# Optimization experiments

Hardware: AMD Instinct MI355X
Metric: run time of the kernel (lower is better)

## Reference

```python
import jax, jax.numpy as jnp
import numpy as np

N = 4096       # nodes
E = 131072     # edges (avg degree 32)
IN_C = 512
HID = 512
OUT_C = 64
RANK = 64      # svd_q
N_DOM = 4
EPS = 1e-5     # BatchNorm eps


def setup_inputs() -> dict:
    key = jax.random.key(0)
    ks = jax.random.split(key, 12)
    x = jax.random.normal(ks[0], (N, IN_C), dtype=jnp.float32)
    row = jax.random.randint(ks[1], (E,), 0, N)
    off = jax.random.randint(ks[2], (E,), 1, N)
    col = (row + off) % N  # guarantee no pre-existing self loops
    edge_index = jnp.stack([row, col]).astype(jnp.int32)
    edge_weight = jax.random.uniform(ks[3], (E,), dtype=jnp.float32)
    y = jax.random.randint(ks[4], (N,), 0, N_DOM).astype(jnp.int32)
    W1 = jax.random.normal(ks[5], (IN_C, HID), dtype=jnp.float32) / np.sqrt(IN_C).astype(np.float32)
    b1 = jnp.zeros((HID,), jnp.float32)
    Wmu = jax.random.normal(ks[6], (HID, OUT_C), dtype=jnp.float32) / np.sqrt(HID).astype(np.float32)
    bmu = jnp.zeros((OUT_C,), jnp.float32)
    Wlv = jax.random.normal(ks[7], (HID, OUT_C), dtype=jnp.float32) / np.sqrt(HID).astype(np.float32)
    blv = jnp.zeros((OUT_C,), jnp.float32)
    gamma = jnp.ones((N_DOM, HID), jnp.float32)   # per-domain BN weight
    beta = jnp.zeros((N_DOM, HID), jnp.float32)   # per-domain BN bias
    return dict(x=x, edge_index=edge_index, edge_weight=edge_weight, y=y,
                W1=W1, b1=b1, Wmu=Wmu, bmu=bmu, Wlv=Wlv, blv=blv,
                gamma=gamma, beta=beta)


def _safe_rsqrt(deg):
    # PyG gcn_norm: deg^-0.5 with inf (and here non-positive) masked to 0
    safe = jnp.where(deg > 0, deg, 1.0)
    return jnp.where(deg > 0, 1.0 / jnp.sqrt(safe), 0.0)


def gcn_conv_edges(x, W, b, row, col, w, n):
    # GCNConv with edge weights: add remaining self loops (fill=1), symmetric norm
    loop = jnp.arange(n, dtype=row.dtype)
    row_f = jnp.concatenate([row, loop])
    col_f = jnp.concatenate([col, loop])
    w_f = jnp.concatenate([w, jnp.ones((n,), w.dtype)])
    deg = jax.ops.segment_sum(w_f, col_f, num_segments=n)
    dinv = _safe_rsqrt(deg)
    norm = dinv[row_f] * w_f * dinv[col_f]
    xw = x @ W                                   # [n, out]
    out = jax.ops.segment_sum(norm[:, None] * xw[row_f], col_f, num_segments=n)
    return out + b


def gcn_conv_dense(x, W, b, A):
    # Dense-adjacency GCNConv (reconstructed adjacency already has a diagonal,
    # so add_remaining_self_loops is a no-op). deg over target (col) index.
    deg = A.sum(axis=0)
    dinv = _safe_rsqrt(deg)
    Ahat = dinv[:, None] * A * dinv[None, :]     # [n, n] normalized
    return Ahat.T @ (x @ W) + b                  # aggregate at targets


def svd_lowrank_recon(A, q, niter=2):
    # torch.svd_lowrank-style randomized SVD, then U @ diag(s) @ V^T
    omega = jax.random.normal(jax.random.key(42), (A.shape[1], q), A.dtype)
    Qb = jnp.linalg.qr(A @ omega)[0]
    for _ in range(niter):
        Qb = jnp.linalg.qr(A.T @ Qb)[0]
        Qb = jnp.linalg.qr(A @ Qb)[0]
    B = Qb.T @ A                                 # [q, n]
    U, s, Vt = jnp.linalg.svd(B, full_matrices=False)
    return (Qb @ (U * s)) @ Vt                   # [n, n] low-rank reconstruction


def dsbn_relu(x, y, gamma, beta):
    # Domain-specific BatchNorm (training-mode batch stats per domain) + ReLU
    out = jnp.zeros_like(x)
    for i in range(N_DOM):
        m = (y == i)
        mf = m.astype(x.dtype)[:, None]
        cnt = jnp.maximum(mf.sum(), 1.0)
        mean = (x * mf).sum(0) / cnt
        var = (((x - mean) ** 2) * mf).sum(0) / cnt   # biased var, as BatchNorm
        xn = (x - mean) / jnp.sqrt(var + EPS) * gamma[i] + beta[i]
        out = jnp.where(m[:, None], xn, out)
    return jax.nn.relu(out)


def reference(x, edge_index, edge_weight, y, W1, b1, Wmu, bmu, Wlv, blv, gamma, beta):
    row, col = edge_index[0], edge_index[1]
    # ----- branch 1: original sparse graph -----
    h1 = dsbn_relu(gcn_conv_edges(x, W1, b1, row, col, edge_weight, N), y, gamma, beta)
    z_mean1 = gcn_conv_edges(h1, Wmu, bmu, row, col, edge_weight, N)
    z_log1 = gcn_conv_edges(h1, Wlv, blv, row, col, edge_weight, N)
    # ----- branch 2: SVD low-rank reconstructed (dense) graph -----
    A = jnp.zeros((N, N), x.dtype).at[row, col].add(edge_weight)  # coalesced COO
    A2 = svd_lowrank_recon(A, RANK)
    h2 = dsbn_relu(gcn_conv_dense(x, W1, b1, A2), y, gamma, beta)
    z_mean2 = gcn_conv_dense(h2, Wmu, bmu, A2)
    z_log2 = gcn_conv_dense(h2, Wlv, blv, A2)
    return (z_mean1, z_log1, z_mean2, z_log2)
```

## Files before the change

kernel.cpp:

```cpp
#include <hip/hip_runtime.h>
#include <hip/hip_bf16.h>


#define NN    4096
#define NEDG  131072
#define INC   512
#define HIDC  512
#define OUTC  64
#define RK    64
#define NDOM  4
#define EPSBN 1e-5f

typedef unsigned short ushortT;
typedef __attribute__((ext_vector_type(8))) short bf16x8;
typedef __attribute__((ext_vector_type(4))) float f32x4;

static inline int cdiv(int a, int b){ return (a + b - 1) / b; }

__device__ __forceinline__ float bf2f(unsigned u){ return __uint_as_float(u << 16); }

__global__ __launch_bounds__(256) void k_detect(const unsigned short* __restrict__ p,
                                                int* __restrict__ flag){
  int t = threadIdx.x;
  int cnt = 0;
// ... 26 lines not shown
#define OFF1 (SEG_X)
#define OFF2 (OFF1+SEG_W1)
#define OFF3 (OFF2+SEG_W)
#define OFF4 (OFF3+SEG_WMU)
#define OFF5 (OFF4+SEG_WMU)
#define OFF6 (OFF5+SEG_GB)
#define OFF7 (OFF6+SEG_GB)
#define OFF8 (OFF7+SEG_B1)
#define OFF9 (OFF8+SEG_BO)
#define OFFT (OFF9+SEG_BO)

__global__ __launch_bounds__(256) void k_upcast_all(
    const void* x, const void* W1, const void* w, const void* Wmu, const void* Wlv,
    const void* gm, const void* bt, const void* b1, const void* bmu, const void* blv,
    const int* __restrict__ isf32,
    float* dx, float* dW1, float* dw, float* dWmu, float* dWlv,
    float* dgm, float* dbt, float* db1, float* dbmu, float* dblv,
    ushortT* xbf, ushortT* W1bf, ushortT* Wmubf, ushortT* Wlvbf){
  int i = blockIdx.x*256 + threadIdx.x;
  if (i >= OFFT) return;
  int f = *isf32;
  if      (i < OFF1){ float v = upc1(x, f, i); dx[i] = v; xbf[i] = tobf(v); }
  else if (i < OFF2){ float v = upc1(W1, f, i - OFF1); dW1[i - OFF1] = v; W1bf[i - OFF1] = tobf(v); }
  else if (i < OFF3) dw  [i - OFF2] = upc1(w,   f, i - OFF2);
  else if (i < OFF4){ float v = upc1(Wmu, f, i - OFF3); dWmu[i - OFF3] = v; Wmubf[i - OFF3] = tobf(v); }
  else if (i < OFF5){ float v = upc1(Wlv, f, i - OFF4); dWlv[i - OFF4] = v; Wlvbf[i - OFF4] = tobf(v); }
  else if (i < OFF6) dgm [i - OFF5] = upc1(gm,  f, i - OFF5);
  else if (i < OFF7) dbt [i - OFF6] = upc1(bt,  f, i - OFF6);
  else if (i < OFF8) db1 [i - OFF7] = upc1(b1,  f, i - OFF7);
  else if (i < OFF9) dbmu[i - OFF8] = upc1(bmu, f, i - OFF8);
  else               dblv[i - OFF9] = upc1(blv, f, i - OFF9);
}

__global__ __launch_bounds__(256) void k_fill(float* d, float v, int n){
  int i = blockIdx.x*256 + threadIdx.x;
  if (i < n) d[i] = v;
}
__global__ __launch_bounds__(256) void k_filld(double* d, double v, int n){
  int i = blockIdx.x*256 + threadIdx.x;
  if (i < n) d[i] = v;
}
__global__ __launch_bounds__(256) void k_prep(float* deg, int* cntR, int* cntC, int* dcnt){
  int i = blockIdx.x*256 + threadIdx.x;
  if (i < NN){ deg[i] = 1.0f; cntR[i] = 0; cntC[i] = 0; }
  if (i < NDOM) dcnt[i] = 0;
}
__global__ __launch_bounds__(256) void k_fin(const double* __restrict__ Qd,
        float* __restrict__ Bf1, const double* __restrict__ Cd, float* __restrict__ Cm,
        const double* __restrict__ qs, float* __restrict__ dinv2){
  int i = blockIdx.x*256 + threadIdx.x;
  if (i < NN*RK){ Bf1[i] = (float)Qd[i]; Cm[i] = (float)Cd[i]; }
  if (i < NN){
    double s = 0.0;
    #pragma unroll
    for (int k = 0; k < RK; k++) s += Cd[(size_t)i*RK + k] * qs[k];
    dinv2[i] = (s > 0.0) ? (float)(1.0/sqrt(s)) : 0.f;
  }
}

__global__ __launch_bounds__(256) void k_hist(const int* __restrict__ row, const int* __restrict__ col,
                                              const float* __restrict__ w, float* deg,
                                              int* cntR, int* cntC){
  int e = blockIdx.x*256 + threadIdx.x;
  if (e < NEDG){
    atomicAdd(&deg[col[e]], w[e]);
    atomicAdd(&cntR[row[e]], 1);
    atomicAdd(&cntC[col[e]], 1);
  }
}
__global__ __launch_bounds__(256) void k_dinv(const float* deg, float* dinv, int n){
  int i = blockIdx.x*256 + threadIdx.x;
  if (i < n){ float d = deg[i]; dinv[i] = (d > 0.f) ? 1.f/sqrtf(d) : 0.f; }
}
__global__ __launch_bounds__(256) void k_norm1(const int* __restrict__ row, const int* __restrict__ col,
                                               const float* __restrict__ w, const float* __restrict__ dinv,
                                               float* __restrict__ nrm){
  int e = blockIdx.x*256 + threadIdx.x;
  if (e < NEDG) nrm[e] = dinv[row[e]] * w[e] * dinv[col[e]];
}
__global__ __launch_bounds__(1024) void k_scan4096(const int* __restrict__ cnt,
                                                   int* __restrict__ ptr, int* __restrict__ pos){
  __shared__ int sh[1024];
  int t = threadIdx.x;
  int b = t*4;
  int a0 = cnt[b], a1 = cnt[b+1], a2 = cnt[b+2], a3 = cnt[b+3];
  sh[t] = a0 + a1 + a2 + a3;
  __syncthreads();
  for (int off = 1; off < 1024; off <<= 1){
    int v = (t >= off) ? sh[t-off] : 0;
    __syncthreads();
// ... 52 lines not shown

__device__ double erfinv64(double x){
  double w = -log1p(-x*x);
  double p;
  if (w < 5.0){
    w -= 2.5;
    p = 2.81022636e-08;  p = p*w + 3.43273939e-07; p = p*w - 3.5233877e-06;
    p = p*w - 4.39150654e-06; p = p*w + 0.00021858087; p = p*w - 0.00125372503;
    p = p*w - 0.00417768164;  p = p*w + 0.246640727;   p = p*w + 1.50140941;
  } else {
    w = sqrt(w) - 3.0;
    p = -0.000200214257; p = p*w + 0.000100950558; p = p*w + 0.00134934322;
    p = p*w - 0.00367342844; p = p*w + 0.00573950773; p = p*w - 0.0076224613;
    p = p*w + 0.00943887047; p = p*w + 1.00167406;    p = p*w + 2.83297682;
  }
  double y = p * x;
  const double c = 1.1283791670955126;
  #pragma unroll
  for (int it = 0; it < 3; it++){
    double err = erf(y) - x;
    y -= err / (c * exp(-y*y));
  }
  return y;
}

__device__ float bits_to_normal(unsigned b){
  float f = __uint_as_float((b >> 9) | 0x3f800000u) - 1.0f;
  const float lo = -0.99999994f;
  float x = fmaxf(lo, f * 2.0f + lo);
  double r = 1.4142135623730951 * erfinv64((double)x);
  return (float)r;
}

__global__ __launch_bounds__(256) void k_omega(float* __restrict__ om){
  int i = blockIdx.x*256 + threadIdx.x;
  if (i >= 262144) return;
  unsigned o0, o1;
  tf2x32(0u, 42u, 0u, (unsigned)i, &o0, &o1);
  om[i] = bits_to_normal(o0 ^ o1);
}

__global__ __launch_bounds__(256) void k_gemm_bf16(
    const ushortT* __restrict__ A, const ushortT* __restrict__ B,
    float* __restrict__ Cc, ushortT* __restrict__ Cbf){
  __shared__ ushortT As2[64][40];
  __shared__ ushortT Bs2[64][40];
  int t = threadIdx.x;
  int bm = blockIdx.y * 64, bn = blockIdx.x * 64;
  int w = t >> 6, l = t & 63;
  int lr = l & 15, lk = l >> 4;
  f32x4 acc[4] = {};
  int ar = t >> 2, ac = (t & 3) * 8;
  int bc = t & 63, bk = (t >> 6) * 8;
  for (int k0 = 0; k0 < 512; k0 += 32){
    *(uint4*)&As2[ar][ac] = *(const uint4*)&A[(size_t)(bm + ar) * 512 + k0 + ac];
    ushortT tmp[8];
    #pragma unroll
    for (int j = 0; j < 8; j++)
      tmp[j] = B[(size_t)(k0 + bk + j) * 512 + bn + bc];
    *(uint4*)&Bs2[bc][bk] = *(uint4*)tmp;
    __syncthreads();
    bf16x8 afrag = *(bf16x8*)&As2[w * 16 + lr][lk * 8];
    #pragma unroll
    for (int nt = 0; nt < 4; nt++){
      bf16x8 bfrag = *(bf16x8*)&Bs2[nt * 16 + lr][lk * 8];
      acc[nt] = __builtin_amdgcn_mfma_f32_16x16x32_bf16(afrag, bfrag, acc[nt], 0, 0, 0);
    }
    __syncthreads();
  }
  #pragma unroll
  for (int nt = 0; nt < 4; nt++){
    #pragma unroll
    for (int i = 0; i < 4; i++){
      size_t idx = (size_t)(bm + w * 16 + lk * 4 + i) * 512 + bn + nt * 16 + lr;
      float v = acc[nt][i];
      Cc[idx] = v;
      Cbf[idx] = tobf(v);
    }
  }
}

__global__ __launch_bounds__(256) void k_gemm_hw2(
    const ushortT* __restrict__ A, const ushortT* __restrict__ Bm,
    const ushortT* __restrict__ Bl, float* __restrict__ Ca, float* __restrict__ Cb){
  __shared__ ushortT As2[64][40];
  __shared__ ushortT Bs2[64][40];
  int t = threadIdx.x;
  int nb = NN/64;
  int second = blockIdx.x >= nb;
  int bm = (blockIdx.x - (second ? nb : 0)) * 64;
  const ushortT* B = second ? Bl : Bm;
  float* Cc = second ? Cb : Ca;
  int w = t >> 6, l = t & 63;
  int lr = l & 15, lk = l >> 4;
  f32x4 acc[4] = {};
  int ar = t >> 2, ac = (t & 3) * 8;
  int bc = t & 63, bk = (t >> 6) * 8;
  for (int k0 = 0; k0 < 512; k0 += 32){
    *(uint4*)&As2[ar][ac] = *(const uint4*)&A[(size_t)(bm + ar) * 512 + k0 + ac];
    ushortT tmp[8];
    #pragma unroll
    for (int j = 0; j < 8; j++)
      tmp[j] = B[(size_t)(k0 + bk + j) * 64 + bc];
    *(uint4*)&Bs2[bc][bk] = *(uint4*)tmp;
    __syncthreads();
    bf16x8 afrag = *(bf16x8*)&As2[w * 16 + lr][lk * 8];
    #pragma unroll
    for (int nt = 0; nt < 4; nt++){
      bf16x8 bfrag = *(bf16x8*)&Bs2[nt * 16 + lr][lk * 8];
      acc[nt] = __builtin_amdgcn_mfma_f32_16x16x32_bf16(afrag, bfrag, acc[nt], 0, 0, 0);
    }
    __syncthreads();
  }
  #pragma unroll
  for (int nt = 0; nt < 4; nt++){
    #pragma unroll
    for (int i = 0; i < 4; i++){
      Cc[(size_t)(bm + w * 16 + lk * 4 + i) * 64 + nt * 16 + lr] = acc[nt][i];
    }
  }
}

__global__ __launch_bounds__(256) void k_gemm_nn(int M, int Nn, int K,
      const float* __restrict__ A, int lda, const float* __restrict__ B, int ldb,
      float* __restrict__ Cc, int ldc, const float* __restrict__ rowscale,
      const float* __restrict__ kscale, const float* __restrict__ bias){
  __shared__ float As[16][65];
  __shared__ float Bs[16][65];
  int bm = blockIdx.y*64, bn = blockIdx.x*64;
  int t = threadIdx.x;
  int tr = t >> 4, tc = t & 15;
  float acc[4][4] = {};
  for (int k0 = 0; k0 < K; k0 += 16){
    #pragma unroll
    for (int q = 0; q < 4; q++){
      int idx = t*4 + q;
      int m = idx >> 4, kk = idx & 15;
      As[kk][m] = A[(size_t)(bm+m)*lda + (k0+kk)];
    }
    #pragma unroll
    for (int q = 0; q < 4; q++){
      int idx = t + q*256;
      int kk = idx >> 6, n = idx & 63;
      float ks = kscale ? kscale[k0+kk] : 1.0f;
      Bs[kk][n] = B[(size_t)(k0+kk)*ldb + (bn+n)] * ks;
    }
    __syncthreads();
    #pragma unroll
    for (int kk = 0; kk < 16; kk++){
      float a0 = As[kk][tr*4+0], a1 = As[kk][tr*4+1], a2 = As[kk][tr*4+2], a3 = As[kk][tr*4+3];
      float b0 = Bs[kk][tc*4+0], b1 = Bs[kk][tc*4+1], b2 = Bs[kk][tc*4+2], b3 = Bs[kk][tc*4+3];
      acc[0][0] += a0*b0; acc[0][1] += a0*b1; acc[0][2] += a0*b2; acc[0][3] += a0*b3;
      acc[1][0] += a1*b0; acc[1][1] += a1*b1; acc[1][2] += a1*b2; acc[1][3] += a1*b3;
      acc[2][0] += a2*b0; acc[2][1] += a2*b1; acc[2][2] += a2*b2; acc[2][3] += a2*b3;
      acc[3][0] += a3*b0; acc[3][1] += a3*b1; acc[3][2] += a3*b2; acc[3][3] += a3*b3;
    }
    __syncthreads();
  }
  #pragma unroll
  for (int i2 = 0; i2 < 4; i2++){
    int m = bm + tr*4 + i2;
    float rs = rowscale ? rowscale[m] : 1.0f;
    #pragma unroll
    for (int j2 = 0; j2 < 4; j2++){
      int n = bn + tc*4 + j2;
      float v = acc[i2][j2] * rs;
      if (bias) v += bias[n];
      Cc[(size_t)m*ldc + n] = v;
    }
  }
}

__global__ __launch_bounds__(256) void k_gemm_nn2(
      const float* __restrict__ A,
      const float* __restrict__ Um,
      const float* __restrict__ rowscale,
      const float* __restrict__ bmu, const float* __restrict__ blv,
      float* __restrict__ zout){
  __shared__ float As[16][65];
  __shared__ float Bs[16][65];
  int z = blockIdx.z;
  const float* B = Um + (size_t)z*RK*RK;
  const float* bias = z ? blv : bmu;
  float* Cc = zout + (size_t)(2+z)*NN*OUTC;
  int bm = blockIdx.y*64;
  int t = threadIdx.x;
  int tr = t >> 4, tc = t & 15;
  float acc[4][4] = {};
  for (int k0 = 0; k0 < RK; k0 += 16){
    #pragma unroll
    for (int q = 0; q < 4; q++){
      int idx = t*4 + q;
      int m = idx >> 4, kk = idx & 15;
      As[kk][m] = A[(size_t)(bm+m)*RK + (k0+kk)];
    }
    #pragma unroll
    for (int q = 0; q < 4; q++){
      int idx = t + q*256;
      int kk = idx >> 6, n = idx & 63;
      Bs[kk][n] = B[(size_t)(k0+kk)*RK + n];
    }
    __syncthreads();
    #pragma unroll
    for (int kk = 0; kk < 16; kk++){
      float a0 = As[kk][tr*4+0], a1 = As[kk][tr*4+1], a2 = As[kk][tr*4+2], a3 = As[kk][tr*4+3];
      float b0 = Bs[kk][tc*4+0], b1 = Bs[kk][tc*4+1], b2 = Bs[kk][tc*4+2], b3 = Bs[kk][tc*4+3];
      acc[0][0] += a0*b0; acc[0][1] += a0*b1; acc[0][2] += a0*b2; acc[0][3] += a0*b3;
      acc[1][0] += a1*b0; acc[1][1] += a1*b1; acc[1][2] += a1*b2; acc[1][3] += a1*b3;
// ... 14 lines not shown
  }
}

__global__ __launch_bounds__(256) void k_gemm_tn_sk(int M, int Nn, int K, int kchunk,
      const float* __restrict__ A, int lda, const float* __restrict__ B, int ldb,
      float* __restrict__ Cc, int ldc, const float* __restrict__ kscale){
  __shared__ float As[32][17];
  __shared__ float Bs[32][17];
  int bm = blockIdx.y*16, bn = blockIdx.x*16;
  int kb = blockIdx.z*kchunk, ke = kb + kchunk;
  int t = threadIdx.x;
  int tm = t >> 4, tn = t & 15;
  float acc = 0.f;
  for (int k0 = kb; k0 < ke; k0 += 32){
    #pragma unroll
    for (int q = 0; q < 2; q++){
      int idx = t + q*256;
      int kk = idx >> 4, m = idx & 15;
      float sv = kscale ? kscale[k0+kk] : 1.0f;
      As[kk][m] = A[(size_t)(k0+kk)*lda + (bm+m)] * sv;
      Bs[kk][m] = B[(size_t)(k0+kk)*ldb + (bn+m)];
    }
    __syncthreads();
    #pragma unroll
    for (int kk = 0; kk < 32; kk++) acc += As[kk][tm] * Bs[kk][tn];
    __syncthreads();
  }
  atomicAdd(&Cc[(size_t)(bm+tm)*ldc + (bn+tn)], acc);
}

__global__ __launch_bounds__(256) void k_gemm_tn_sk2(
      const float* __restrict__ A,
      const float* __restrict__ Ba, const float* __restrict__ Bb,
      float* __restrict__ Um,
      const float* __restrict__ kscale){
  __shared__ float As[32][17];
  __shared__ float Bs[32][17];
  int z = blockIdx.z;
  int second = z >= 16;
  int kb = (second ? z - 16 : z) * 256, ke = kb + 256;
  const float* B = second ? Bb : Ba;
  float* Cc = Um + (second ? RK*RK : 0);
  int bm = blockIdx.y*16, bn = blockIdx.x*16;
  int t = threadIdx.x;
  int tm = t >> 4, tn = t & 15;
  float acc = 0.f;
  for (int k0 = kb; k0 < ke; k0 += 32){
    #pragma unroll
    for (int q = 0; q < 2; q++){
      int idx = t + q*256;
      int kk = idx >> 4, m = idx & 15;
      As[kk][m] = A[(size_t)(k0+kk)*RK + (bm+m)] * kscale[k0+kk];
      Bs[kk][m] = B[(size_t)(k0+kk)*OUTC + (bn+m)];
    }
    __syncthreads();
    #pragma unroll
    for (int kk = 0; kk < 32; kk++) acc += As[kk][tm] * Bs[kk][tn];
    __syncthreads();
  }
  atomicAdd(&Cc[(size_t)(bm+tm)*RK + (bn+tn)], acc);
}

__global__ __launch_bounds__(64) void k_spmm32(const int* __restrict__ ptr,
                       const int* __restrict__ src, const float* __restrict__ cf,
                       const float* __restrict__ X, float* __restrict__ Y){
  int seg = blockIdx.x;
  int t = threadIdx.x;
  double acc = 0.0;
  int p0 = ptr[seg], p1 = ptr[seg+1];
  for (int p = p0; p < p1; ++p){
    acc += (double)cf[p] * (double)X[(size_t)src[p]*RK + t];
  }
  Y[(size_t)seg*RK + t] = (float)acc;
}
__global__ __launch_bounds__(64) void k_spmm32to64(const int* __restrict__ ptr,
                       const int* __restrict__ src, const float* __restrict__ cf,
                       const float* __restrict__ X, double* __restrict__ Y){
  int seg = blockIdx.x;
  int t = threadIdx.x;
  double acc = 0.0;
  int p0 = ptr[seg], p1 = ptr[seg+1];
  for (int p = p0; p < p1; ++p){
    acc += (double)cf[p] * (double)X[(size_t)src[p]*RK + t];
  }
  Y[(size_t)seg*RK + t] = acc;
}
__global__ __launch_bounds__(64) void k_spmm64(const int* __restrict__ ptr,
                       const int* __restrict__ src, const float* __restrict__ cf,
                       const double* __restrict__ X, double* __restrict__ Y){
  int seg = blockIdx.x;
  int t = threadIdx.x;
  double acc = 0.0;
  int p0 = ptr[seg], p1 = ptr[seg+1];
  for (int p = p0; p < p1; ++p){
    acc += (double)cf[p] * X[(size_t)src[p]*RK + t];
  }
  Y[(size_t)seg*RK + t] = acc;
}
__global__ __launch_bounds__(256) void k_gram64(const double* __restrict__ X, double* __restrict__ G){
  __shared__ double Xs[64][65];
  int b = blockIdx.x;
  int t = threadIdx.x;
  #pragma unroll
  for (int q = 0; q < 16; q++){
    int idx = t + q*256;
    Xs[idx >> 6][idx & 63] = X[(size_t)(b*64 + (idx >> 6))*RK + (idx & 63)];
  }
  __syncthreads();
  int i = t >> 2;
  int j0 = (t & 3) * 16;
  double acc[16];
  #pragma unroll
  for (int jj = 0; jj < 16; jj++) acc[jj] = 0.0;
  for (int k = 0; k < 64; k++){
    double a = Xs[k][i];
    #pragma unroll
    for (int jj = 0; jj < 16; jj++) acc[jj] += a * Xs[k][j0+jj];
  }
  #pragma unroll
  for (int jj = 0; jj < 16; jj++) atomicAdd(&G[i*RK + j0 + jj], acc[jj]);
}

#define CHOLF_CHUNK(I0) \
  for (int k2 = 0; k2 < 16; k2++){ \
    int k = (I0) + k2; \
    int buf = k & 1; \
    if (t < 64 && j == k){ \
      double d = sqrt(fmax(cdiag, 1e-300)); \
// ... 36 lines not shown
    CHOLF_CHUNK(48)
    if (t < 64){
      #pragma unroll
      for (int i = 0; i < 64; i++){
        double v = (i > j) ? c[i] : 0.0;
        if (i == j) v = myd;
        G[i*64 + j] = v;
      }
    }
  } else {
    int seg = blockIdx.x - 1;
    float acc0, acc1;
    {
      float sd = self_dinv[seg]; float s2 = sd*sd;
      unsigned v = *(const unsigned*)&Xb[(size_t)seg*HIDC + 2*t];
      acc0 = s2 * bf2f(v & 0xffffu);
      acc1 = s2 * bf2f(v >> 16);
    }
    int p0 = ptr[seg], p1 = ptr[seg+1];
    for (int p = p0; p < p1; ++p){
      int o = src[p];
      float cc = cf[p];
      unsigned v = *(const unsigned*)&Xb[(size_t)o*HIDC + 2*t];
      acc0 += cc * bf2f(v & 0xffffu);
      acc1 += cc * bf2f(v >> 16);
    }
    acc0 += bias[2*t];
    acc1 += bias[2*t+1];
    Y[(size_t)seg*HIDC + 2*t]     = acc0;
    Y[(size_t)seg*HIDC + 2*t + 1] = acc1;
  }
}

__global__ __launch_bounds__(256) void k_trinv64(const double* __restrict__ L,
      const double* __restrict__ sdd, double* __restrict__ Rinv){
  __shared__ double gl[64][65];
  __shared__ double Xl[64][65];
  __shared__ double sdinv[64];
  __shared__ double Sl[3][16][17];
  int t = threadIdx.x;
  #pragma unroll
  for (int q = 0; q < 16; q++){
    int idx = t + (q << 8);
    gl[idx >> 6][idx & 63] = L[idx];
  }
  if (t < 64) sdinv[t] = sdd[t];
  for (int idx = t; idx < 64*65; idx += 256)
    ((double*)Xl)[idx] = 0.0;
  __syncthreads();
  if (t < 64){
    int b = t >> 4, c2 = t & 15;
    int g0 = b << 4;
    int gc = g0 + c2;
    Xl[gc][gc] = sdinv[gc];
    for (int i = c2 - 1; i >= 0; i--){
      int gi = g0 + i;
      double s = 0.0;
      for (int k2 = i + 1; k2 <= c2; k2++)
        s += gl[g0 + k2][gi] * Xl[g0 + k2][gc];
      Xl[gi][gc] = -s * sdinv[gi];
    }
  }
  __syncthreads();
  for (int d = 1; d < 4; d++){
    int np = 4 - d;
    int tot = np << 8;
    for (int e = t; e < tot; e += 256){
      int p = e >> 8;
      int i = (e >> 4) & 15, jj = e & 15;
      int gi = (p << 4) + i, gj = ((p + d) << 4) + jj;
      double s = 0.0;
      int a0 = (p + 1) << 4, a1 = (p + d + 1) << 4;
      for (int a = a0; a < a1; a++)
        s += gl[a][gi] * Xl[a][gj];
      Sl[p][i][jj] = s;
    }
    __syncthreads();
    for (int e = t; e < tot; e += 256){
      int p = e >> 8;
      int i = (e >> 4) & 15, jj = e & 15;
      int gi = (p << 4) + i, gj = ((p + d) << 4) + jj;
      double s = 0.0;
      #pragma unroll
      for (int k2 = 0; k2 < 16; k2++)
        s += Xl[gi][(p << 4) + k2] * Sl[p][k2][jj];
      Xl[gi][gj] = -s;
    }
    __syncthreads();
  }
  #pragma unroll
  for (int q = 0; q < 16; q++){
    int e2 = t + (q << 8);
    Rinv[e2] = Xl[e2 >> 6][e2 & 63];
  }
}
__global__ __launch_bounds__(256) void k_applyR64(const double* __restrict__ src,
      const double* __restrict__ Rinv, double* __restrict__ dst){
  __shared__ double Rs[64][65];
  int t = threadIdx.x;
  #pragma unroll
  for (int q = 0; q < 16; q++){
    int idx = t + q*256;
    Rs[idx >> 6][idx & 63] = Rinv[idx];
  }
  __syncthreads();
  int r = blockIdx.x*4 + (t >> 6);
  int j = t & 63;
  const double* rowp = src + (size_t)r*RK;
  double s = 0.0;
  for (int k = 0; k <= j; k++) s += rowp[k] * Rs[k][j];
  dst[(size_t)r*RK + j] = s;
}
__global__ __launch_bounds__(256) void k_qsum64(const double* __restrict__ Q, double* __restrict__ qs){
  int j = blockIdx.x;  int t = threadIdx.x;
  double a = 0.0;
  for (int n = t; n < NN; n += 256) a += Q[(size_t)n*RK + j];
  __shared__ double sh[256];
  sh[t] = a; __syncthreads();
  for (int off = 128; off > 0; off >>= 1){ if (t < off) sh[t] += sh[t+off]; __syncthreads(); }
  if (t == 0) qs[j] = sh[0];
}

__global__ void k_spmm2(const int* __restrict__ ptr, const int* __restrict__ src,
                        const float* __restrict__ cf,
                        const float* __restrict__ Xa, const float* __restrict__ Xb2,
                        float* __restrict__ zout,
                        const float* __restrict__ self_dinv,
                        const float* __restrict__ bmu, const float* __restrict__ blv){
  int b = blockIdx.x;
  int second = b >= NN;
  int seg = second ? b - NN : b;
  const float* X = second ? Xb2 : Xa;
  const float* bias = second ? blv : bmu;
  float* Y = zout + (second ? (size_t)NN*OUTC : 0);
  int t = threadIdx.x;
  float acc0;
  {
    float sd = self_dinv[seg];
    acc0 = sd*sd * X[(size_t)seg*OUTC + t];
  }
  int p0 = ptr[seg], p1 = ptr[seg+1];
  for (int p = p0; p < p1; ++p){
    acc0 += cf[p] * X[(size_t)src[p]*OUTC + t];
  }
  acc0 += bias[t];
  Y[(size_t)seg*OUTC + t] = acc0;
}

__global__ __launch_bounds__(256) void k_bnstats(const float* __restrict__ H, const int* __restrict__ y,
        const int* __restrict__ dcnt, const float* __restrict__ gamma, const float* __restrict__ beta,
        float* __restrict__ scal, float* __restrict__ shft){
  int j = blockIdx.x;
  int t = threadIdx.x;
  float s0=0,s1=0,s2=0,s3=0,q0=0,q1=0,q2=0,q3=0;
  for (int n = t; n < NN; n += 256){
    float v = H[(size_t)n*HIDC + j];
    int d = y[n];
    float v2 = v*v;
    if      (d == 0){ s0 += v; q0 += v2; }
    else if (d == 1){ s1 += v; q1 += v2; }
    else if (d == 2){ s2 += v; q2 += v2; }
    else            { s3 += v; q3 += v2; }
  }
  __shared__ float sh[256][8];
  sh[t][0]=s0; sh[t][1]=s1; sh[t][2]=s2; sh[t][3]=s3;
  sh[t][4]=q0; sh[t][5]=q1; sh[t][6]=q2; sh[t][7]=q3;
  __syncthreads();
  for (int off = 128; off > 0; off >>= 1){
    if (t < off){
      #pragma unroll
      for (int q = 0; q < 8; q++) sh[t][q] += sh[t+off][q];
    }
    __syncthreads();
  }
  if (t < NDOM){
    float cnt  = fmaxf((float)dcnt[t], 1.0f);
    float mean = sh[0][t] / cnt;
    float var  = fmaxf(sh[0][4+t] / cnt - mean*mean, 0.f);
    float inv  = 1.0f / sqrtf(var + EPSBN);
    float gmm  = gamma[t*HIDC + j];
    scal[t*HIDC + j] = gmm * inv;
    shft[t*HIDC + j] = beta[t*HIDC + j] - mean * gmm * inv;
  }
}
__global__ __launch_bounds__(256) void k_bnapply(float* __restrict__ H, const int* __restrict__ y,
        const float* __restrict__ scal, const float* __restrict__ shft,
        ushortT* __restrict__ Hbf){
  int idx = blockIdx.x*256 + threadIdx.x;
  if (idx >= NN*HIDC) return;
  int n = idx >> 9, j = idx & (HIDC-1);
  int d = y[n];
  float v = H[idx] * scal[d*HIDC + j] + shft[d*HIDC + j];
  v = v > 0.f ? v : 0.f;
  H[idx] = v;
  Hbf[idx] = tobf(v);
}

extern "C" void kernel_launch(void* const* d_in, const int* in_sizes, int n_in,
                              void* d_out, int out_size, void* d_ws, size_t ws_size,
                              hipStream_t stream){
  (void)in_sizes; (void)n_in; (void)out_size;
  const void* x_in  = d_in[0];
  const int*  ei    = (const int*)d_in[1];
  const void* w_in  = d_in[2];
  const int*  yv    = (const int*)d_in[3];
  const void* W1i   = d_in[4];
  const void* b1i   = d_in[5];
  const void* Wmui  = d_in[6];
  const void* bmui  = d_in[7];
  const void* Wlvi  = d_in[8];
  const void* blvi  = d_in[9];
  const void* gmi   = d_in[10];
  const void* bti   = d_in[11];
  const int* rowA = ei;
  const int* colA = ei + NEDG;
  float* zout = (float*)d_out;

  double* Dp = (double*)d_ws;
  size_t od = 0;
  double* Qd0 = Dp + od; od += (size_t)NN*RK;
  double* Qd1 = Dp + od; od += (size_t)NN*RK;
  double* Cd  = Dp + od; od += (size_t)NN*RK;
  double* Gd  = Dp + od; od += RK*RK;
  double* Rid = Dp + od; od += RK*RK;
  double* qsd = Dp + od; od += RK;
  double* sdd = Dp + od; od += RK;
  float* Fp = (float*)(Dp + od);
  size_t o = 0;
  float* xf   = Fp + o; o += (size_t)NN*INC;
  float* W1f  = Fp + o; o += (size_t)INC*HIDC;
  float* b1f  = Fp + o; o += HIDC;
  float* Wmuf = Fp + o; o += (size_t)HIDC*OUTC;
  float* bmuf = Fp + o; o += OUTC;
  float* Wlvf = Fp + o; o += (size_t)HIDC*OUTC;
  float* blvf = Fp + o; o += OUTC;
  float* gmf  = Fp + o; o += NDOM*HIDC;
  float* btf  = Fp + o; o += NDOM*HIDC;
  float* wf   = Fp + o; o += NEDG;
  float* xw1  = Fp + o; o += (size_t)NN*HIDC;
  float* hwA  = Fp + o; o += (size_t)NN*OUTC;
  float* hwB  = Fp + o; o += (size_t)NN*OUTC;
  float* Bf1  = Fp + o; o += (size_t)NN*RK;
  float* Cm   = Fp + o; o += (size_t)NN*RK;
  float* Qf0  = Fp + o; o += (size_t)NN*RK;
  float* Qf1  = Fp + o; o += (size_t)NN*RK;
  float* Tm   = Fp + o; o += (size_t)RK*HIDC;
  float* Umu  = Fp + o; o += 2*RK*RK;
  float* deg1 = Fp + o; o += NN;
  float* dinv1= Fp + o; o += NN;
  float* dinv2= Fp + o; o += NN;
  float* norm1= Fp + o; o += NEDG;
  float* scal = Fp + o; o += NDOM*HIDC;
  float* shft = Fp + o; o += NDOM*HIDC;
  float* csrW = Fp + o; o += NEDG;
  float* cscW = Fp + o; o += NEDG;
  float* cscN = Fp + o; o += NEDG;
  ushortT* xbf   = (ushortT*)(Fp + o); o += (size_t)NN*INC/2;
  ushortT* W1bf  = (ushortT*)(Fp + o); o += (size_t)INC*HIDC/2;
  ushortT* xw1bf = (ushortT*)(Fp + o); o += (size_t)NN*HIDC/2;
  ushortT* hbf   = (ushortT*)(Fp + o); o += (size_t)NN*HIDC/2;
  ushortT* Wmubf = (ushortT*)(Fp + o); o += (size_t)HIDC*OUTC/2;
  ushortT* Wlvbf = (ushortT*)(Fp + o); o += (size_t)HIDC*OUTC/2;
  int* Ip = (int*)(Fp + o);
  size_t oi = 0;
  int* cntR = Ip + oi; oi += NN;
  int* ptrR = Ip + oi; oi += NN + 1;
  int* posR = Ip + oi; oi += NN;
  int* eidR = Ip + oi; oi += NEDG;
  int* cntC = Ip + oi; oi += NN;
  int* ptrC = Ip + oi; oi += NN + 1;
  int* posC = Ip + oi; oi += NN;
  int* eidC = Ip + oi; oi += NEDG;
  int* csrSrc = Ip + oi; oi += NEDG;
  int* cscSrc = Ip + oi; oi += NEDG;
  int* dcnt = Ip + oi; oi += NDOM;
  int* dflag= Ip + oi; oi += 1;

  size_t need = od*sizeof(double) + o*sizeof(float) + (oi+16)*sizeof(int);
  if (ws_size < need) return;

  float* hbuf = xf;

  const int T = 256;
  k_detect<<<1,T,0,stream>>>((const unsigned short*)x_in, dflag);
  k_upcast_all<<<cdiv(OFFT,T),T,0,stream>>>(
      x_in, W1i, w_in, Wmui, Wlvi, gmi, bti, b1i, bmui, blvi, dflag,
      xf, W1f, wf, Wmuf, Wlvf, gmf, btf, b1f, bmuf, blvf,
      xbf, W1bf, Wmubf, Wlvbf);

  k_prep<<<cdiv(NN,T),T,0,stream>>>(deg1, cntR, cntC, dcnt);
  k_hist <<<cdiv(NEDG,T),T,0,stream>>>(rowA, colA, wf, deg1, cntR, cntC);
  k_dinv <<<cdiv(NN,T),T,0,stream>>>(deg1, dinv1, NN);
  k_norm1<<<cdiv(NEDG,T),T,0,stream>>>(rowA, colA, wf, dinv1, norm1);
  k_scan4096<<<1,1024,0,stream>>>(cntR, ptrR, posR);
  k_scan4096<<<1,1024,0,stream>>>(cntC, ptrC, posC);
  k_scatter<<<cdiv(NEDG,T),T,0,stream>>>(rowA, colA, posR, posC, eidR, eidC);
  k_edges<<<cdiv(NEDG,T),T,0,stream>>>(rowA, colA, wf, norm1, eidR, eidC,
                                       csrSrc, csrW, cscSrc, cscW, cscN);
  k_omega<<<cdiv(NN*RK,T),T,0,stream>>>(Qf0);
  k_dcnt <<<cdiv(NN,T),T,0,stream>>>(yv, dcnt);

  k_gemm_bf16<<<dim3(HIDC/64, NN/64),256,0,stream>>>(xbf, W1bf, xw1, xw1bf);

  k_spmm32<<<NN,64,0,stream>>>(ptrR, csrSrc, csrW, Qf0, Qf1);
  k_spmm32<<<NN,64,0,stream>>>(ptrC, cscSrc, cscW, Qf1, Qf0);
  k_spmm32<<<NN,64,0,stream>>>(ptrR, csrSrc, csrW, Qf0, Qf1);
  k_spmm32<<<NN,64,0,stream>>>(ptrC, cscSrc, cscW, Qf1, Qf0);
  k_spmm32to64<<<NN,64,0,stream>>>(ptrR, csrSrc, csrW, Qf0, Qd1);
  k_filld<<<cdiv(RK*RK,T),T,0,stream>>>(Gd, 0.0, RK*RK);
  k_gram64<<<NN/64,256,0,stream>>>(Qd1, Gd);

  k_chol_spmm<<<NN+1,256,0,stream>>>(Gd, sdd, ptrC, cscSrc, cscN, xw1bf, hbuf,
                                     dinv1, b1f);

  k_trinv64<<<1,256,0,stream>>>(Gd, sdd, Rid);
  k_applyR64<<<NN/4,256,0,stream>>>(Qd1, Rid, Qd0);
  k_spmm64<<<NN,64,0,stream>>>(ptrC, cscSrc, cscW, Qd0, Cd);
  k_qsum64<<<RK,256,0,stream>>>(Qd0, qsd);
  k_fin<<<cdiv(NN*RK,T),T,0,stream>>>(Qd0, Bf1, Cd, Cm, qsd, dinv2);

  k_bnstats<<<HIDC,256,0,stream>>>(hbuf, yv, dcnt, gmf, btf, scal, shft);
  k_bnapply<<<cdiv(NN*HIDC,T),T,0,stream>>>(hbuf, yv, scal, shft, hbf);
  k_gemm_hw2<<<2*(NN/64),256,0,stream>>>(hbf, Wmubf, Wlvbf, hwA, hwB);
  k_spmm2<<<2*NN,64,0,stream>>>(ptrC, cscSrc, cscN, hwA, hwB, zout, dinv1, bmuf, blvf);

  k_fill<<<cdiv(RK*HIDC,T),T,0,stream>>>(Tm, 0.f, RK*HIDC);
  k_gemm_tn_sk<<<dim3(HIDC/16, RK/16, 8),256,0,stream>>>(RK,HIDC,NN,512, Bf1,RK, xw1,HIDC, Tm,HIDC, dinv2);
  k_gemm_nn<<<dim3(HIDC/64, NN/64),256,0,stream>>>(NN,HIDC,RK, Cm,RK, Tm,HIDC, hbuf,HIDC, dinv2, nullptr, b1f);
  k_bnstats<<<HIDC,256,0,stream>>>(hbuf, yv, dcnt, gmf, btf, scal, shft);
  k_bnapply<<<cdiv(NN*HIDC,T),T,0,stream>>>(hbuf, yv, scal, shft, hbf);
  k_gemm_hw2<<<2*(NN/64),256,0,stream>>>(hbf, Wmubf, Wlvbf, hwA, hwB);
  k_fill<<<cdiv(2*RK*RK,T),T,0,stream>>>(Umu, 0.f, 2*RK*RK);
  k_gemm_tn_sk2<<<dim3(RK/16, RK/16, 32),256,0,stream>>>(Bf1, hwA, hwB, Umu, dinv2);
  k_gemm_nn2<<<dim3(1, NN/64, 2),256,0,stream>>>(Cm, Umu, dinv2, bmuf, blvf, zout);
}
```

Before: 578.1 us.

## Merge independent kernels into shared launches and rewrite BatchNorm stats via atomics

Removes the separate fill kernels by folding their zeroing into existing kernels (k_omega, k_prep, k_fin). Independent stages of the SVD branch and the sparse branch (triangular inverse, applyR, spmm64, qsum) now share launches with BN partial sums, BN apply, the hw2 GEMM and spmm2, using block-index dispatch. BN statistics are computed as row-blocked partial sums accumulated with atomics, and scale/shift are folded into the apply step. The aim is to cut launch count and the serialized single-block tails. In exchange, float atomics make the sums non-deterministic, and the mixed kernels carry the register and shared-memory footprint of their heaviest path.

Measured after the change: 556.3 us. -3.8%, faster.

```diff
diff --git a/kernel.cpp b/kernel.cpp
--- a/kernel.cpp
+++ b/kernel.cpp
@@ -82,22 +82,17 @@
   else               dblv[i - OFF9] = upc1(blv, f, i - OFF9);
 }
 
-__global__ __launch_bounds__(256) void k_fill(float* d, float v, int n){
-  int i = blockIdx.x*256 + threadIdx.x;
-  if (i < n) d[i] = v;
-}
-__global__ __launch_bounds__(256) void k_filld(double* d, double v, int n){
-  int i = blockIdx.x*256 + threadIdx.x;
-  if (i < n) d[i] = v;
-}
-__global__ __launch_bounds__(256) void k_prep(float* deg, int* cntR, int* cntC, int* dcnt){
+__global__ __launch_bounds__(256) void k_prep(float* deg, int* cntR, int* cntC, int* dcnt,
+                                              float* bnsum){
   int i = blockIdx.x*256 + threadIdx.x;
   if (i < NN){ deg[i] = 1.0f; cntR[i] = 0; cntC[i] = 0; }
   if (i < NDOM) dcnt[i] = 0;
+  if (i < 8*HIDC) bnsum[i] = 0.f;
 }
 __global__ __launch_bounds__(256) void k_fin(const double* __restrict__ Qd,
         float* __restrict__ Bf1, const double* __restrict__ Cd, float* __restrict__ Cm,
-        const double* __restrict__ qs, float* __restrict__ dinv2){
+        const double* __restrict__ qs, float* __restrict__ dinv2,
+        float* __restrict__ Tm, float* __restrict__ Um, float* __restrict__ bnsum){
   int i = blockIdx.x*256 + threadIdx.x;
   if (i < NN*RK){ Bf1[i] = (float)Qd[i]; Cm[i] = (float)Cd[i]; }
   if (i < NN){
@@ -106,6 +101,9 @@
     for (int k = 0; k < RK; k++) s += Cd[(size_t)i*RK + k] * qs[k];
     dinv2[i] = (s > 0.0) ? (float)(1.0/sqrt(s)) : 0.f;
   }
+  if (i < RK*HIDC) Tm[i] = 0.f;
+  if (i < 2*RK*RK) Um[i] = 0.f;
+  if (i < 8*HIDC)  bnsum[i] = 0.f;
 }
 
 __global__ __launch_bounds__(256) void k_hist(const int* __restrict__ row, const int* __restrict__ col,
@@ -224,8 +222,9 @@
   return (float)r;
 }
 
-__global__ __launch_bounds__(256) void k_omega(float* __restrict__ om){
+__global__ __launch_bounds__(256) void k_omega(float* __restrict__ om, double* __restrict__ Gd){
   int i = blockIdx.x*256 + threadIdx.x;
+  if (i < RK*RK) Gd[i] = 0.0;
   if (i >= 262144) return;
   unsigned o0, o1;
   tf2x32(0u, 42u, 0u, (unsigned)i, &o0, &o1);
@@ -272,15 +271,14 @@
   }
 }
 
-__global__ __launch_bounds__(256) void k_gemm_hw2(
+__device__ __forceinline__ void d_hw2(int bx, int t,
     const ushortT* __restrict__ A, const ushortT* __restrict__ Bm,
     const ushortT* __restrict__ Bl, float* __restrict__ Ca, float* __restrict__ Cb){
   __shared__ ushortT As2[64][40];
   __shared__ ushortT Bs2[64][40];
-  int t = threadIdx.x;
   int nb = NN/64;
-  int second = blockIdx.x >= nb;
-  int bm = (blockIdx.x - (second ? nb : 0)) * 64;
+  int second = bx >= nb;
+  int bm = (bx - (second ? nb : 0)) * 64;
   const ushortT* B = second ? Bl : Bm;
   float* Cc = second ? Cb : Ca;
   int w = t >> 6, l = t & 63;
@@ -312,6 +310,11 @@
     }
   }
 }
+__global__ __launch_bounds__(256) void k_gemm_hw2(
+    const ushortT* __restrict__ A, const ushortT* __restrict__ Bm,
+    const ushortT* __restrict__ Bl, float* __restrict__ Ca, float* __restrict__ Cb){
+  d_hw2(blockIdx.x, threadIdx.x, A, Bm, Bl, Ca, Cb);
+}
 
 __global__ __launch_bounds__(256) void k_gemm_nn(int M, int Nn, int K,
       const float* __restrict__ A, int lda, const float* __restrict__ B, int ldb,
@@ -364,8 +367,7 @@
 }
 
 __global__ __launch_bounds__(256) void k_gemm_nn2(
-      const float* __restrict__ A,
-      const float* __restrict__ Um,
+      const float* __restrict__ A, const float* __restrict__ Um,
       const float* __restrict__ rowscale,
       const float* __restrict__ bmu, const float* __restrict__ blv,
       float* __restrict__ zout){
@@ -446,8 +448,7 @@
 __global__ __launch_bounds__(256) void k_gemm_tn_sk2(
       const float* __restrict__ A,
       const float* __restrict__ Ba, const float* __restrict__ Bb,
-      float* __restrict__ Um,
-      const float* __restrict__ kscale){
+      float* __restrict__ Um, const float* __restrict__ kscale){
   __shared__ float As[32][17];
   __shared__ float Bs[32][17];
   int z = blockIdx.z;
@@ -496,18 +497,6 @@
   int p0 = ptr[seg], p1 = ptr[seg+1];
   for (int p = p0; p < p1; ++p){
     acc += (double)cf[p] * (double)X[(size_t)src[p]*RK + t];
-  }
-  Y[(size_t)seg*RK + t] = acc;
-}
-__global__ __launch_bounds__(64) void k_spmm64(const int* __restrict__ ptr,
-                       const int* __restrict__ src, const float* __restrict__ cf,
-                       const double* __restrict__ X, double* __restrict__ Y){
-  int seg = blockIdx.x;
-  int t = threadIdx.x;
-  double acc = 0.0;
-  int p0 = ptr[seg], p1 = ptr[seg+1];
-  for (int p = p0; p < p1; ++p){
-    acc += (double)cf[p] * X[(size_t)src[p]*RK + t];
   }
   Y[(size_t)seg*RK + t] = acc;
 }
@@ -610,13 +599,75 @@
   }
 }
 
-__global__ __launch_bounds__(256) void k_trinv64(const double* __restrict__ L,
-      const double* __restrict__ sdd, double* __restrict__ Rinv){
+__device__ __forceinline__ void d_bnpart(int b, int t,
+    const float* __restrict__ H, const int* __restrict__ y, float* __restrict__ bnsum){
+  int j0 = 2*t;
+  float s00=0,s01=0,s10=0,s11=0,s20=0,s21=0,s30=0,s31=0;
+  float q00=0,q01=0,q10=0,q11=0,q20=0,q21=0,q30=0,q31=0;
+  int r0 = b*32;
+  for (int r = r0; r < r0+32; r++){
+    int d = y[r];
+    float2 v = *(const float2*)&H[(size_t)r*HIDC + j0];
+    float ax = v.x, ay = v.y;
+    float bx = ax*ax, by = ay*ay;
+    if      (d == 0){ s00+=ax; s01+=ay; q00+=bx; q01+=by; }
+    else if (d == 1){ s10+=ax; s11+=ay; q10+=bx; q11+=by; }
+    else if (d == 2){ s20+=ax; s21+=ay; q20+=bx; q21+=by; }
+    else            { s30+=ax; s31+=ay; q30+=bx; q31+=by; }
+  }
+  atomicAdd(&bnsum[0*HIDC+j0], s00); atomicAdd(&bnsum[0*HIDC+j0+1], s01);
+  atomicAdd(&bnsum[1*HIDC+j0], s10); atomicAdd(&bnsum[1*HIDC+j0+1], s11);
+  atomicAdd(&bnsum[2*HIDC+j0], s20); atomicAdd(&bnsum[2*HIDC+j0+1], s21);
+  atomicAdd(&bnsum[3*HIDC+j0], s30); atomicAdd(&bnsum[3*HIDC+j0+1], s31);
+  atomicAdd(&bnsum[4*HIDC+j0], q00); atomicAdd(&bnsum[4*HIDC+j0+1], q01);
+  atomicAdd(&bnsum[5*HIDC+j0], q10); atomicAdd(&bnsum[5*HIDC+j0+1], q11);
+  atomicAdd(&bnsum[6*HIDC+j0], q20); atomicAdd(&bnsum[6*HIDC+j0+1], q21);
+  atomicAdd(&bnsum[7*HIDC+j0], q30); atomicAdd(&bnsum[7*HIDC+j0+1], q31);
+}
+__global__ __launch_bounds__(256) void k_bnpart(const float* __restrict__ H,
+        const int* __restrict__ y, float* __restrict__ bnsum){
+  d_bnpart(blockIdx.x, threadIdx.x, H, y, bnsum);
+}
+
+__device__ __forceinline__ void d_bnapply(int idx,
+    float* __restrict__ H, const int* __restrict__ y,
+    const float* __restrict__ bnsum, const int* __restrict__ dcnt,
+    const float* __restrict__ gamma, const float* __restrict__ beta,
+    ushortT* __restrict__ Hbf){
+  int n = idx >> 9, j = idx & (HIDC-1);
+  int d = y[n];
+  float cnt  = fmaxf((float)dcnt[d], 1.0f);
+  float mean = bnsum[d*HIDC + j] / cnt;
+  float var  = fmaxf(bnsum[(4+d)*HIDC + j] / cnt - mean*mean, 0.f);
+  float inv  = 1.0f / sqrtf(var + EPSBN);
+  float gmm  = gamma[d*HIDC + j];
+  float scal = gmm * inv;
+  float shft = beta[d*HIDC + j] - mean * gmm * inv;
+  float v = H[idx] * scal + shft;
+  v = v > 0.f ? v : 0.f;
+  H[idx] = v;
+  Hbf[idx] = tobf(v);
+}
+__global__ __launch_bounds__(256) void k_bnapply(float* __restrict__ H, const int* __restrict__ y,
+        const float* __restrict__ bnsum, const int* __restrict__ dcnt,
+        const float* __restrict__ gamma, const float* __restrict__ beta,
+        ushortT* __restrict__ Hbf){
+  int idx = blockIdx.x*256 + threadIdx.x;
+  if (idx < NN*HIDC) d_bnapply(idx, H, y, bnsum, dcnt, gamma, beta, Hbf);
+}
+
+__global__ __launch_bounds__(256) void k_trinv_bn(const double* __restrict__ L,
+      const double* __restrict__ sdd, double* __restrict__ Rinv,
+      const float* __restrict__ H, const int* __restrict__ y, float* __restrict__ bnsum){
+  int t = threadIdx.x;
+  if (blockIdx.x > 0){
+    d_bnpart(blockIdx.x - 1, t, H, y, bnsum);
+    return;
+  }
   __shared__ double gl[64][65];
   __shared__ double Xl[64][65];
   __shared__ double sdinv[64];
   __shared__ double Sl[3][16][17];
-  int t = threadIdx.x;
   #pragma unroll
   for (int q = 0; q < 16; q++){
     int idx = t + (q << 8);
@@ -672,10 +723,20 @@
     Rinv[e2] = Xl[e2 >> 6][e2 & 63];
   }
 }
-__global__ __launch_bounds__(256) void k_applyR64(const double* __restrict__ src,
-      const double* __restrict__ Rinv, double* __restrict__ dst){
+
+__global__ __launch_bounds__(256) void k_applyR_bn(const double* __restrict__ srcQ,
+      const double* __restrict__ Rinv, double* __restrict__ dst,
+      float* __restrict__ H, const int* __restrict__ y,
+      const float* __restrict__ bnsum, const int* __restrict__ dcnt,
+      const float* __restrict__ gamma, const float* __restrict__ beta,
+      ushortT* __restrict__ Hbf){
+  int t = threadIdx.x;
+  if (blockIdx.x >= NN/4){
+    int idx = (blockIdx.x - NN/4)*256 + t;
+    if (idx < NN*HIDC) d_bnapply(idx, H, y, bnsum, dcnt, gamma, beta, Hbf);
+    return;
+  }
   __shared__ double Rs[64][65];
-  int t = threadIdx.x;
   #pragma unroll
   for (int q = 0; q < 16; q++){
     int idx = t + q*256;
@@ -684,94 +745,67 @@
   __syncthreads();
   int r = blockIdx.x*4 + (t >> 6);
   int j = t & 63;
-  const double* rowp = src + (size_t)r*RK;
+  const double* rowp = srcQ + (size_t)r*RK;
   double s = 0.0;
   for (int k = 0; k <= j; k++) s += rowp[k] * Rs[k][j];
   dst[(size_t)r*RK + j] = s;
 }
-__global__ __launch_bounds__(256) void k_qsum64(const double* __restrict__ Q, double* __restrict__ qs){
-  int j = blockIdx.x;  int t = threadIdx.x;
-  double a = 0.0;
-  for (int n = t; n < NN; n += 256) a += Q[(size_t)n*RK + j];
-  __shared__ double sh[256];
-  sh[t] = a; __syncthreads();
-  for (int off = 128; off > 0; off >>= 1){ if (t < off) sh[t] += sh[t+off]; __syncthreads(); }
-  if (t == 0) qs[j] = sh[0];
-}
-
-__global__ void k_spmm2(const int* __restrict__ ptr, const int* __restrict__ src,
-                        const float* __restrict__ cf,
-                        const float* __restrict__ Xa, const float* __restrict__ Xb2,
-                        float* __restrict__ zout,
-                        const float* __restrict__ self_dinv,
-                        const float* __restrict__ bmu, const float* __restrict__ blv){
-  int b = blockIdx.x;
-  int second = b >= NN;
-  int seg = second ? b - NN : b;
+
+__global__ __launch_bounds__(256) void k_spmmC_hw2(
+    const int* __restrict__ ptr, const int* __restrict__ src, const float* __restrict__ cf,
+    const double* __restrict__ X, double* __restrict__ Y,
+    const ushortT* __restrict__ A, const ushortT* __restrict__ Bm,
+    const ushortT* __restrict__ Bl, float* __restrict__ Ca, float* __restrict__ Cb){
+  int t = threadIdx.x;
+  if (blockIdx.x >= NN/4){
+    d_hw2(blockIdx.x - NN/4, t, A, Bm, Bl, Ca, Cb);
+    return;
+  }
+  int seg = blockIdx.x*4 + (t >> 6);
+  int lane = t & 63;
+  double acc = 0.0;
+  int p0 = ptr[seg], p1 = ptr[seg+1];
+  for (int p = p0; p < p1; ++p){
+    acc += (double)cf[p] * X[(size_t)src[p]*RK + lane];
+  }
+  Y[(size_t)seg*RK + lane] = acc;
+}
+
+__global__ __launch_bounds__(256) void k_qsum_spmm2(
+    const double* __restrict__ Q, double* __restrict__ qs,
+    const int* __restrict__ ptr, const int* __restrict__ src, const float* __restrict__ cf,
+    const float* __restrict__ Xa, const float* __restrict__ Xb2,
+    float* __restrict__ zout, const float* __restrict__ self_dinv,
+    const float* __restrict__ bmu, const float* __restrict__ blv){
+  int t = threadIdx.x;
+  if (blockIdx.x < 64){
+    int j = blockIdx.x;
+    double a = 0.0;
+    for (int n = t; n < NN; n += 256) a += Q[(size_t)n*RK + j];
+    __shared__ double sh[256];
+    sh[t] = a; __syncthreads();
+    for (int off = 128; off > 0; off >>= 1){ if (t < off) sh[t] += sh[t+off]; __syncthreads(); }
+    if (t == 0) qs[j] = sh[0];
+    return;
+  }
+  int bb = blockIdx.x - 64;
+  int second = bb >= NN/4;
+  int seg = (second ? bb - NN/4 : bb)*4 + (t >> 6);
+  int lane = t & 63;
   const float* X = second ? Xb2 : Xa;
   const float* bias = second ? blv : bmu;
   float* Y = zout + (second ? (size_t)NN*OUTC : 0);
-  int t = threadIdx.x;
   float acc0;
   {
     float sd = self_dinv[seg];
-    acc0 = sd*sd * X[(size_t)seg*OUTC + t];
+    acc0 = sd*sd * X[(size_t)seg*OUTC + lane];
   }
   int p0 = ptr[seg], p1 = ptr[seg+1];
   for (int p = p0; p < p1; ++p){
-    acc0 += cf[p] * X[(size_t)src[p]*OUTC + t];
-  }
-  acc0 += bias[t];
-  Y[(size_t)seg*OUTC + t] = acc0;
-}
-
-__global__ __launch_bounds__(256) void k_bnstats(const float* __restrict__ H, const int* __restrict__ y,
-        const int* __restrict__ dcnt, const float* __restrict__ gamma, const float* __restrict__ beta,
-        float* __restrict__ scal, float* __restrict__ shft){
-  int j = blockIdx.x;
-  int t = threadIdx.x;
-  float s0=0,s1=0,s2=0,s3=0,q0=0,q1=0,q2=0,q3=0;
-  for (int n = t; n < NN; n += 256){
-    float v = H[(size_t)n*HIDC + j];
-    int d = y[n];
-    float v2 = v*v;
-    if      (d == 0){ s0 += v; q0 += v2; }
-    else if (d == 1){ s1 += v; q1 += v2; }
-    else if (d == 2){ s2 += v; q2 += v2; }
-    else            { s3 += v; q3 += v2; }
-  }
-  __shared__ float sh[256][8];
-  sh[t][0]=s0; sh[t][1]=s1; sh[t][2]=s2; sh[t][3]=s3;
-  sh[t][4]=q0; sh[t][5]=q1; sh[t][6]=q2; sh[t][7]=q3;
-  __syncthreads();
-  for (int off = 128; off > 0; off >>= 1){
-    if (t < off){
-      #pragma unroll
-      for (int q = 0; q < 8; q++) sh[t][q] += sh[t+off][q];
-    }
-    __syncthreads();
-  }
-  if (t < NDOM){
-    float cnt  = fmaxf((float)dcnt[t], 1.0f);
-    float mean = sh[0][t] / cnt;
-    float var  = fmaxf(sh[0][4+t] / cnt - mean*mean, 0.f);
-    float inv  = 1.0f / sqrtf(var + EPSBN);
-    float gmm  = gamma[t*HIDC + j];
-    scal[t*HIDC + j] = gmm * inv;
-    shft[t*HIDC + j] = beta[t*HIDC + j] - mean * gmm * inv;
-  }
-}
-__global__ __launch_bounds__(256) void k_bnapply(float* __restrict__ H, const int* __restrict__ y,
-        const float* __restrict__ scal, const float* __restrict__ shft,
-        ushortT* __restrict__ Hbf){
-  int idx = blockIdx.x*256 + threadIdx.x;
-  if (idx >= NN*HIDC) return;
-  int n = idx >> 9, j = idx & (HIDC-1);
-  int d = y[n];
-  float v = H[idx] * scal[d*HIDC + j] + shft[d*HIDC + j];
-  v = v > 0.f ? v : 0.f;
-  H[idx] = v;
-  Hbf[idx] = tobf(v);
+    acc0 += cf[p] * X[(size_t)src[p]*OUTC + lane];
+  }
+  acc0 += bias[lane];
+  Y[(size_t)seg*OUTC + lane] = acc0;
 }
 
 extern "C" void kernel_launch(void* const* d_in, const int* in_sizes, int n_in,
@@ -828,8 +862,7 @@
   float* dinv1= Fp + o; o += NN;
   float* dinv2= Fp + o; o += NN;
   float* norm1= Fp + o; o += NEDG;
-  float* scal = Fp + o; o += NDOM*HIDC;
-  float* shft = Fp + o; o += NDOM*HIDC;
+  float* bnsum= Fp + o; o += 8*HIDC;
   float* csrW = Fp + o; o += NEDG;
   float* cscW = Fp + o; o += NEDG;
   float* cscN = Fp + o; o += NEDG;
@@ -866,7 +899,7 @@
       xf, W1f, wf, Wmuf, Wlvf, gmf, btf, b1f, bmuf, blvf,
       xbf, W1bf, Wmubf, Wlvbf);
 
-  k_prep<<<cdiv(NN,T),T,0,stream>>>(deg1, cntR, cntC, dcnt);
+  k_prep<<<cdiv(NN,T),T,0,stream>>>(deg1, cntR, cntC, dcnt, bnsum);
   k_hist <<<cdiv(NEDG,T),T,0,stream>>>(rowA, colA, wf, deg1, cntR, cntC);
   k_dinv <<<cdiv(NN,T),T,0,stream>>>(deg1, dinv1, NN);
   k_norm1<<<cdiv(NEDG,T),T,0,stream>>>(rowA, colA, wf, dinv1, norm1);
@@ -875,7 +908,7 @@
   k_scatter<<<cdiv(NEDG,T),T,0,stream>>>(rowA, colA, posR, posC, eidR, eidC);
   k_edges<<<cdiv(NEDG,T),T,0,stream>>>(rowA, colA, wf, norm1, eidR, eidC,
                                        csrSrc, csrW, cscSrc, cscW, cscN);
-  k_omega<<<cdiv(NN*RK,T),T,0,stream>>>(Qf0);
+  k_omega<<<cdiv(NN*RK,T),T,0,stream>>>(Qf0, Gd);
   k_dcnt <<<cdiv(NN,T),T,0,stream>>>(yv, dcnt);
 
   k_gemm_bf16<<<dim3(HIDC/64, NN/64),256,0,stream>>>(xbf, W1bf, xw1, xw1bf);
@@ -885,30 +918,24 @@
   k_spmm32<<<NN,64,0,stream>>>(ptrR, csrSrc, csrW, Qf0, Qf1);
   k_spmm32<<<NN,64,0,stream>>>(ptrC, cscSrc, cscW, Qf1, Qf0);
   k_spmm32to64<<<NN,64,0,stream>>>(ptrR, csrSrc, csrW, Qf0, Qd1);
-  k_filld<<<cdiv(RK*RK,T),T,0,stream>>>(Gd, 0.0, RK*RK);
   k_gram64<<<NN/64,256,0,stream>>>(Qd1, Gd);
 
   k_chol_spmm<<<NN+1,256,0,stream>>>(Gd, sdd, ptrC, cscSrc, cscN, xw1bf, hbuf,
                                      dinv1, b1f);
-
-  k_trinv64<<<1,256,0,stream>>>(Gd, sdd, Rid);
-  k_applyR64<<<NN/4,256,0,stream>>>(Qd1, Rid, Qd0);
-  k_spmm64<<<NN,64,0,stream>>>(ptrC, cscSrc, cscW, Qd0, Cd);
-  k_qsum64<<<RK,256,0,stream>>>(Qd0, qsd);
-  k_fin<<<cdiv(NN*RK,T),T,0,stream>>>(Qd0, Bf1, Cd, Cm, qsd, dinv2);
-
-  k_bnstats<<<HIDC,256,0,stream>>>(hbuf, yv, dcnt, gmf, btf, scal, shft);
-  k_bnapply<<<cdiv(NN*HIDC,T),T,0,stream>>>(hbuf, yv, scal, shft, hbf);
-  k_gemm_hw2<<<2*(NN/64),256,0,stream>>>(hbf, Wmubf, Wlvbf, hwA, hwB);
-  k_spmm2<<<2*NN,64,0,stream>>>(ptrC, cscSrc, cscN, hwA, hwB, zout, dinv1, bmuf, blvf);
-
-  k_fill<<<cdiv(RK*HIDC,T),T,0,stream>>>(Tm, 0.f, RK*HIDC);
+  k_trinv_bn<<<1+NN/32,256,0,stream>>>(Gd, sdd, Rid, hbuf, yv, bnsum);
+  k_applyR_bn<<<NN/4 + cdiv(NN*HIDC,T),256,0,stream>>>(Qd1, Rid, Qd0,
+      hbuf, yv, bnsum, dcnt, gmf, btf, hbf);
+  k_spmmC_hw2<<<NN/4 + 2*(NN/64),256,0,stream>>>(ptrC, cscSrc, cscW, Qd0, Cd,
+      hbf, Wmubf, Wlvbf, hwA, hwB);
+  k_qsum_spmm2<<<64 + 2*(NN/4),256,0,stream>>>(Qd0, qsd, ptrC, cscSrc, cscN,
+      hwA, hwB, zout, dinv1, bmuf, blvf);
+  k_fin<<<cdiv(NN*RK,T),T,0,stream>>>(Qd0, Bf1, Cd, Cm, qsd, dinv2, Tm, Umu, bnsum);
+
   k_gemm_tn_sk<<<dim3(HIDC/16, RK/16, 8),256,0,stream>>>(RK,HIDC,NN,512, Bf1,RK, xw1,HIDC, Tm,HIDC, dinv2);
   k_gemm_nn<<<dim3(HIDC/64, NN/64),256,0,stream>>>(NN,HIDC,RK, Cm,RK, Tm,HIDC, hbuf,HIDC, dinv2, nullptr, b1f);
-  k_bnstats<<<HIDC,256,0,stream>>>(hbuf, yv, dcnt, gmf, btf, scal, shft);
-  k_bnapply<<<cdiv(NN*HIDC,T),T,0,stream>>>(hbuf, yv, scal, shft, hbf);
+  k_bnpart<<<NN/32,256,0,stream>>>(hbuf, yv, bnsum);
+  k_bnapply<<<cdiv(NN*HIDC,T),T,0,stream>>>(hbuf, yv, bnsum, dcnt, gmf, btf, hbf);
   k_gemm_hw2<<<2*(NN/64),256,0,stream>>>(hbf, Wmubf, Wlvbf, hwA, hwB);
-  k_fill<<<cdiv(2*RK*RK,T),T,0,stream>>>(Umu, 0.f, 2*RK*RK);
   k_gemm_tn_sk2<<<dim3(RK/16, RK/16, 32),256,0,stream>>>(Bf1, hwA, hwB, Umu, dinv2);
   k_gemm_nn2<<<dim3(1, NN/64, 2),256,0,stream>>>(Cm, Umu, dinv2, bmuf, blvf, zout);
 }
```
